# Optimization experiments

Measured on AMD Instinct MI355X. Metric: run time of the kernel, lower is better.

## Reference

```python
import jax, jax.numpy as jnp
import numpy as np


def setup_inputs() -> dict:
    key = jax.random.key(0)
    k1, k2, k3 = jax.random.split(key, 3)
    Q, N, D = 2048, 100000, 512
    x = jax.random.normal(k1, (Q, D), dtype=jnp.float32)
    target_embeddings = jax.random.normal(k2, (N, D), dtype=jnp.float32)
    target_labels = jax.random.randint(k3, (N,), 0, 400, dtype=jnp.int64)
    return {"x": x, "target_embeddings": target_embeddings,
            "target_labels": target_labels, "k": 5}


def reference(x, target_embeddings, target_labels, k):
    # torch.cdist(x[:,None], T[None], p=2).squeeze(1): full [Q, N] euclidean distances
    x2 = jnp.sum(x * x, axis=-1, keepdims=True)            # [Q, 1]
    t2 = jnp.sum(target_embeddings * target_embeddings, axis=-1)  # [N]
    d2 = x2 + t2[None, :] - 2.0 * (x @ target_embeddings.T)       # [Q, N]
    dist = jnp.sqrt(jnp.maximum(d2, 0.0))
    # topk smallest distances
    neg_vals, topk_inds = jax.lax.top_k(-dist, k)           # [Q, k]
    topk_dists = -neg_vals
    # pred = target_labels[inds].t() in the original eval path
    pred = target_labels[topk_inds].T                       # [k, Q]
    return topk_dists, topk_inds, pred
```

## Files before the change

### kernel.cpp

```cpp
#include <hip/hip_runtime.h>
#include <float.h>
#include <math.h>

#define NQ 2048
#define NT 100000
#define DIM 512
#define KTOP 5
#define NCAND 16
#define QTILE 128
#define TTILE 128
#define NTPC 13
#define NCH 64
#define TBLKS 782
#define QBLKS 16
#define NSUB 3
#define CV_TBLKS (TBLKS*16)
#define CV_XBLKS ((NQ/128)*16)

typedef float f32x4 __attribute__((ext_vector_type(4)));
typedef short s16x8 __attribute__((ext_vector_type(8)));
typedef unsigned int u32;
typedef unsigned short u16;

__device__ __forceinline__ int tsub_start(int ts) { return (13 * ts + 2) / 3; }

__device__ __forceinline__ bool lt_pair(float v1, int i1, float v2, int i2) {
  return v1 < v2 || (v1 == v2 && i1 < i2);
}

__device__ __forceinline__ void ins5f(float* tv, int* tix, float sc, int idx) {
  if (sc < tv[4]) {
    tv[4] = sc; tix[4] = idx;
#pragma unroll
    for (int p = 4; p > 0; --p)
      if (tv[p] < tv[p - 1]) {
        float tf = tv[p]; tv[p] = tv[p - 1]; tv[p - 1] = tf;
        int tn = tix[p]; tix[p] = tix[p - 1]; tix[p - 1] = tn;
      }
  }
}

__device__ __forceinline__ void ins5(float* tv, int* tix, float sc, int idx) {
  if (lt_pair(sc, idx, tv[4], tix[4])) {
    tv[4] = sc; tix[4] = idx;
#pragma unroll
    for (int p = 4; p > 0; --p)
      if (lt_pair(tv[p], tix[p], tv[p - 1], tix[p - 1])) {
        float tf = tv[p]; tv[p] = tv[p - 1]; tv[p - 1] = tf;
        int tn = tix[p]; tix[p] = tix[p - 1]; tix[p - 1] = tn;
      }
  }
}

__device__ __forceinline__ void merge5(float* av, int* ai, const float* bv, const int* bi) {
  float nv[5]; int ni[5];
#pragma unroll
  for (int s = 0; s < 5; ++s) {
    if (lt_pair(av[s], ai[s], bv[4 - s], bi[4 - s])) { nv[s] = av[s]; ni[s] = ai[s]; }
    else { nv[s] = bv[4 - s]; ni[s] = bi[4 - s]; }
  }
#pragma unroll
  for (int a = 0; a < 5; ++a)
#pragma unroll
    for (int b = 0; b < 4 - a; ++b)
      if (lt_pair(nv[b + 1], ni[b + 1], nv[b], ni[b])) {
        float tf = nv[b]; nv[b] = nv[b + 1]; nv[b + 1] = tf;
        int tn = ni[b]; ni[b] = ni[b + 1]; ni[b + 1] = tn;
      }
#pragma unroll
  for (int s = 0; s < 5; ++s) { av[s] = nv[s]; ai[s] = ni[s]; }
}

__global__ __launch_bounds__(256) void convert_kernel(
    const float* __restrict__ x, const float* __restrict__ T,
    short* __restrict__ xhi, short* __restrict__ thi,
    float* __restrict__ t2, float* __restrict__ x2) {
  __shared__ short lh[4096];
  const int bid = blockIdx.x;
  const bool isT = bid < CV_TBLKS;
  const int task = isT ? bid : bid - CV_TBLKS;
  const int blk = task >> 4, kbi = task & 15;
  const float* src = isT ? T : x;
  short* dhi = isT ? thi : xhi;
  float* nrm = isT ? t2 : x2;
  const int nsrc = isT ? NT : NQ;

  const int t = threadIdx.x;
  const int rr = t >> 1, half = t & 1;
  const int grow = blk * 128 + rr;
  const int rs = grow < nsrc ? grow : nsrc - 1;
  const float* p = src + (size_t)rs * DIM + kbi * 32 + half * 16;
  f32x4 v[4];
#pragma unroll
  for (int i = 0; i < 4; ++i) v[i] = ((const f32x4*)p)[i];

  float ss = 0.f;
#pragma unroll
  for (int g = 0; g < 2; ++g) {
    s16x8 hv;
#pragma unroll
    for (int e = 0; e < 8; ++e) {
      int i = g * 8 + e;
      float f = v[i >> 2][i & 3];
      ss = fmaf(f, f, ss);
      u32 u = __builtin_bit_cast(u32, f);
      u32 r1 = u + 0x7FFFu + ((u >> 16) & 1u);
      hv[e] = (short)(r1 >> 16);
    }
    int unit = (rr >> 4) * 64 + (half * 2 + g) * 16 + (rr & 15);
    *(s16x8*)(lh + unit * 8) = hv;
  }
  ss += __shfl_xor(ss, 1, 64);
  if (half == 0 && grow < nsrc) atomicAdd(nrm + grow, ss);

  __syncthreads();
  size_t obase = ((size_t)(blk * 16 + kbi)) * 4096 + t * 16;
  *(s16x8*)(dhi + obase)     = *(const s16x8*)(lh + t * 16);
  *(s16x8*)(dhi + obase + 8) = *(const s16x8*)(lh + t * 16 + 8);
}

__global__ __launch_bounds__(256, 2) void knn_mfma(
    const short* __restrict__ xhi, const short* __restrict__ thi,
    const float* __restrict__ t2g,
    float* __restrict__ pvals, u16* __restrict__ pidx16) {
  __shared__ float msv[128 * 5];
  __shared__ int   msi[128 * 5];

  const int tid = threadIdx.x;
  const int w = tid >> 6;
  const int l = tid & 63;
  const int bid = blockIdx.x;
  const u32 rest = (u32)bid >> 3;
  const int inner = (int)(rest % 48u);
  const int chunk = (bid & 7) + 8 * (int)(rest / 48u);
  const int qblk = inner & 15;
  const int tsub = inner >> 4;
  const int tstart = tsub_start(tsub);
  const int tend = tsub_start(tsub + 1);
  const int q0 = qblk * QTILE;
  const int wr = (w >> 1) * 64;
  const int wc = (w & 1) * 64;
  const int arow = wr >> 4;
  const int bcol = wc >> 4;

  const s16x8* xh8 = (const s16x8*)xhi;
  const s16x8* th8 = (const s16x8*)thi;

  float tv4[4][KTOP]; int tix4[4][KTOP];
#pragma unroll
  for (int jj = 0; jj < 4; ++jj)
#pragma unroll
    for (int s = 0; s < KTOP; ++s) { tv4[jj][s] = FLT_MAX; tix4[jj][s] = 0x7FFFFFFF; }

#pragma unroll 1
  for (int tt = tstart; tt < tend; ++tt) {
    const int bblk = chunk * NTPC + tt;
    if (bblk >= TBLKS) continue;
    const int tbase = bblk * TTILE;
    f32x4 acc[4][4];
#pragma unroll
    for (int i = 0; i < 4; ++i)
#pragma unroll
      for (int j = 0; j < 4; ++j) acc[i][j] = (f32x4){0.f, 0.f, 0.f, 0.f};

    u32 offA = (u32)(bblk * 16) * 512u + (u32)(arow * 64 + l);
    u32 offB = (u32)(qblk * 16) * 512u + (u32)(bcol * 64 + l);
    s16x8 ah[4], bh[4];
#pragma unroll 1
    for (int kbi = 0; kbi < 16; ++kbi) {
#pragma unroll
      for (int i = 0; i < 4; ++i) {
        ah[i] = th8[offA + i * 64];
        bh[i] = xh8[offB + i * 64];
      }
      offA += 512; offB += 512;
      __builtin_amdgcn_s_setprio(1);
#pragma unroll
      for (int j = 0; j < 4; ++j)
#pragma unroll
        for (int i = 0; i < 4; ++i)
          acc[i][j] = __builtin_amdgcn_mfma_f32_16x16x32_bf16(ah[i], bh[j], acc[i][j], 0, 0, 0);
      __builtin_amdgcn_s_setprio(0);
    }

    const int tg0 = tbase + wr + ((l >> 4) << 2);
    float t2v[16];
#pragma unroll
    for (int i = 0; i < 4; ++i)
#pragma unroll
      for (int r = 0; r < 4; ++r) {
        int t = tg0 + i * 16 + r;
        float vv = t2g[t < NT ? t : NT - 1];
        t2v[i * 4 + r] = t < NT ? vv : FLT_MAX;
      }
#pragma unroll
    for (int jj = 0; jj < 4; ++jj)
#pragma unroll
      for (int i = 0; i < 4; ++i)
#pragma unroll
        for (int r = 0; r < 4; ++r) {
          float sc = fmaf(-2.f, acc[i][jj][r], t2v[i * 4 + r]);
          ins5f(tv4[jj], tix4[jj], sc, tg0 + i * 16 + r);
        }
  }

#pragma unroll
  for (int jj = 0; jj < 4; ++jj)
#pragma unroll
    for (int d = 16; d <= 32; d <<= 1) {
      float ov[KTOP]; int oi[KTOP];
#pragma unroll
      for (int s = 0; s < KTOP; ++s) {
        ov[s] = __shfl_xor(tv4[jj][s], d, 64);
        oi[s] = __shfl_xor(tix4[jj][s], d, 64);
      }
      merge5(tv4[jj], tix4[jj], ov, oi);
    }

  const int blockBase = (chunk * NTPC + tstart) * TTILE;
  if ((w >> 1) && (l >> 4) == 0) {
#pragma unroll
    for (int jj = 0; jj < 4; ++jj) {
      int qr = wc + jj * 16 + l;
#pragma unroll
      for (int s = 0; s < KTOP; ++s) {
        msv[qr * 5 + s] = tv4[jj][s];
        msi[qr * 5 + s] = tix4[jj][s];
      }
    }
  }
  __syncthreads();
  if (!(w >> 1) && (l >> 4) == 0) {
#pragma unroll
    for (int jj = 0; jj < 4; ++jj) {
      int qr = wc + jj * 16 + l;
      float ov[KTOP]; int oi[KTOP];
#pragma unroll
      for (int s = 0; s < KTOP; ++s) { ov[s] = msv[qr * 5 + s]; oi[s] = msi[qr * 5 + s]; }
      merge5(tv4[jj], tix4[jj], ov, oi);
      int q = q0 + qr;
      size_t base = ((size_t)q * (NCH * NSUB) + (chunk * NSUB + tsub)) * KTOP;
#pragma unroll
      for (int s = 0; s < KTOP; ++s) {
        pvals[base + s] = tv4[jj][s];
        pidx16[base + s] = (u16)(tix4[jj][s] - blockBase);
      }
    }
  }
}

__global__ __launch_bounds__(256) void knn_merge16(
    const float* __restrict__ pvals, const u16* __restrict__ pidx16,
    int* __restrict__ idx16g) {
  const int M = NCH * NSUB * KTOP;
  int q = (blockIdx.x * 256 + threadIdx.x) >> 6;
  int l = threadIdx.x & 63;
  if (q >= NQ) return;
  float v[15]; int ix[15];
  size_t base = (size_t)q * M;
#pragma unroll
  for (int j = 0; j < 15; ++j) {
    int m = j * 64 + l;
    int slot = m / KTOP;
    int ch = slot / NSUB, ts = slot % NSUB;
    int gb = (ch * NTPC + tsub_start(ts)) * TTILE;
    v[j] = pvals[base + m];
    ix[j] = gb + (int)pidx16[base + m];
  }
  int mywin = 0x7FFFFFFF;
#pragma unroll 1
  for (int r = 0; r < NCAND; ++r) {
    float bv = FLT_MAX; int bi = 0x7FFFFFFF;
#pragma unroll
    for (int j = 0; j < 15; ++j)
      if (lt_pair(v[j], ix[j], bv, bi)) { bv = v[j]; bi = ix[j]; }
#pragma unroll
    for (int d = 1; d < 64; d <<= 1) {
      float ov = __shfl_xor(bv, d, 64);
      int oi = __shfl_xor(bi, d, 64);
      if (lt_pair(ov, oi, bv, bi)) { bv = ov; bi = oi; }
    }
    if (l == r) mywin = bi;
#pragma unroll
    for (int j = 0; j < 15; ++j)
      if (ix[j] == bi) v[j] = FLT_MAX;
  }
  if (l < NCAND) idx16g[q * NCAND + l] = mywin;
}

__global__ __launch_bounds__(256) void knn_rerank(
    const float* __restrict__ x, const float* __restrict__ T,
    const int* __restrict__ idx16g, const int* __restrict__ labels,
    float* __restrict__ out) {
  __shared__ float sd2[4 * NCAND];
  __shared__ int sti[4 * NCAND];
  const int w = threadIdx.x >> 6, l = threadIdx.x & 63;
  const int q = blockIdx.x * 4 + w;
  const int cand = l >> 2, sub = l & 3;
  const int ti = idx16g[q * NCAND + cand];
  const f32x4* tp = (const f32x4*)(T + (size_t)ti * DIM + sub * 128);
  const f32x4* xp = (const f32x4*)(x + (size_t)q * DIM + sub * 128);
  float dot = 0.f, tt = 0.f, xx = 0.f;
#pragma unroll
  for (int i = 0; i < 32; ++i) {
    f32x4 a = xp[i], b = tp[i];
#pragma unroll
    for (int c = 0; c < 4; ++c) {
      dot = fmaf(a[c], b[c], dot);
      tt  = fmaf(b[c], b[c], tt);
      xx  = fmaf(a[c], a[c], xx);
    }
  }
#pragma unroll
  for (int d = 1; d < 4; d <<= 1) {
    dot += __shfl_xor(dot, d, 64);
    tt  += __shfl_xor(tt, d, 64);
    xx  += __shfl_xor(xx, d, 64);
  }
  if (sub == 0) { sd2[w * NCAND + cand] = xx + tt - 2.f * dot; sti[w * NCAND + cand] = ti; }
  __syncthreads();
  if (l == 0) {
    float tv[KTOP]; int tix[KTOP];
#pragma unroll
    for (int s = 0; s < KTOP; ++s) { tv[s] = FLT_MAX; tix[s] = 0x7FFFFFFF; }
#pragma unroll
    for (int c = 0; c < NCAND; ++c) ins5(tv, tix, sd2[w * NCAND + c], sti[w * NCAND + c]);
#pragma unroll
    for (int s = 0; s < KTOP; ++s) {
      float d2 = tv[s] > 0.f ? tv[s] : 0.f;
      out[(size_t)q * KTOP + s] = sqrtf(d2);
      out[(size_t)NQ * KTOP + (size_t)q * KTOP + s] = (float)tix[s];
      out[(size_t)2 * NQ * KTOP + (size_t)s * NQ + q] =
          (float)labels[tix[s]];
    }
  }
}

extern "C" void kernel_launch(void* const* d_in, const int* in_sizes, int n_in,
                              void* d_out, int out_size, void* d_ws, size_t ws_size,
                              hipStream_t stream) {
  const float* x = (const float*)d_in[0];
  const float* T = (const float*)d_in[1];
  const int* labels = (const int*)d_in[2];
  float* out = (float*)d_out;
  char* ws = (char*)d_ws;

  float* t2     = (float*)(ws + 0);
  float* x2     = (float*)(ws + 401408);
  short* xhi    = (short*)(ws + 409600);
  short* thi    = (short*)(ws + 2506752);
  float* pvals  = (float*)(ws + 105005056);
  u16*   pidx16 = (u16*)(ws + 112869376);
  int*   idx16g = (int*)(ws + 116801536);

  hipMemsetAsync(ws, 0, 409600, stream);

  convert_kernel<<<CV_TBLKS + CV_XBLKS, 256, 0, stream>>>(
      x, T, xhi, thi, t2, x2);

  knn_mfma<<<QBLKS * NSUB * NCH, 256, 0, stream>>>(
      xhi, thi, t2, pvals, pidx16);

  knn_merge16<<<(NQ * 64 + 255) / 256, 256, 0, stream>>>(pvals, pidx16, idx16g);

  knn_rerank<<<NQ / 4, 256, 0, stream>>>(x, T, idx16g, labels, out);
}
```

Measured before the change: 693.1 us.

## Stage MFMA operands through double-buffered LDS via direct global-to-LDS loads

The inner K loop no longer loads bf16 operand fragments from global memory straight into registers. Each block now copies 128x32 tiles of T and X into a two-slot LDS buffer with global_load_lds, overlapping the load of the next k-slice with MFMA on the current one. Each operand is fetched from global once per block and shared across waves, where before each wave loaded its own slice. In exchange the kernel adds 32KB of LDS per block and two __syncthreads per k-step, which may cut occupancy (launch bounds ask for 2 blocks/CU) and drops the s_setprio hints.

New measurement: 809.5 us. +16.8%, slower.

```diff
diff --git a/kernel.cpp b/kernel.cpp
--- a/kernel.cpp
+++ b/kernel.cpp
@@ -123,8 +123,10 @@
     const short* __restrict__ xhi, const short* __restrict__ thi,
     const float* __restrict__ t2g,
     float* __restrict__ pvals, u16* __restrict__ pidx16) {
-  __shared__ float msv[128 * 5];
-  __shared__ int   msi[128 * 5];
+  __shared__ char smem[32768];
+  s16x8 (*stg)[1024] = (s16x8 (*)[1024])smem;
+  float* msv = (float*)smem;
+  int*   msi = (int*)(smem + 2560);
 
   const int tid = threadIdx.x;
   const int w = tid >> 6;
@@ -143,8 +145,34 @@
   const int arow = wr >> 4;
   const int bcol = wc >> 4;
 
-  const s16x8* xh8 = (const s16x8*)xhi;
-  const s16x8* th8 = (const s16x8*)thi;
+#define STAGE_KBI(kbi, b) do {                                                \
+    _Pragma("unroll")                                                         \
+    for (int c = 0; c < 4; ++c) {                                             \
+      int seg = w * 4 + c;                                                    \
+      const short* gsrc = (seg < 8)                                           \
+        ? thi + (((size_t)(bblk * 16 + (kbi))) << 12) + (seg << 9) + (l << 3) \
+        : xhi + (((size_t)(qblk * 16 + (kbi))) << 12) + ((seg - 8) << 9) + (l << 3); \
+      __builtin_amdgcn_global_load_lds(                                       \
+          (const __attribute__((address_space(1))) unsigned int*)gsrc,        \
+          (__attribute__((address_space(3))) unsigned int*)&stg[(b)][seg * 64], \
+          16, 0, 0);                                                          \
+    }                                                                         \
+  } while (0)
+
+#define READ_MFMA(b) do {                                                     \
+    s16x8 ah[4], bh[4];                                                       \
+    _Pragma("unroll")                                                         \
+    for (int i = 0; i < 4; ++i) {                                             \
+      ah[i] = stg[(b)][(arow + i) * 64 + l];                                  \
+      bh[i] = stg[(b)][512 + (bcol + i) * 64 + l];                            \
+    }                                                                         \
+    _Pragma("unroll")                                                         \
+    for (int j = 0; j < 4; ++j)                                               \
+      _Pragma("unroll")                                                       \
+      for (int i = 0; i < 4; ++i)                                             \
+        acc[i][j] = __builtin_amdgcn_mfma_f32_16x16x32_bf16(ah[i], bh[j],     \
+                                                            acc[i][j], 0, 0, 0); \
+  } while (0)
 
   float tv4[4][KTOP]; int tix4[4][KTOP];
 #pragma unroll
@@ -163,24 +191,17 @@
 #pragma unroll
       for (int j = 0; j < 4; ++j) acc[i][j] = (f32x4){0.f, 0.f, 0.f, 0.f};
 
-    u32 offA = (u32)(bblk * 16) * 512u + (u32)(arow * 64 + l);
-    u32 offB = (u32)(qblk * 16) * 512u + (u32)(bcol * 64 + l);
-    s16x8 ah[4], bh[4];
+    STAGE_KBI(0, 0);
+    __syncthreads();
 #pragma unroll 1
-    for (int kbi = 0; kbi < 16; ++kbi) {
-#pragma unroll
-      for (int i = 0; i < 4; ++i) {
-        ah[i] = th8[offA + i * 64];
-        bh[i] = xh8[offB + i * 64];
-      }
-      offA += 512; offB += 512;
-      __builtin_amdgcn_s_setprio(1);
-#pragma unroll
-      for (int j = 0; j < 4; ++j)
-#pragma unroll
-        for (int i = 0; i < 4; ++i)
-          acc[i][j] = __builtin_amdgcn_mfma_f32_16x16x32_bf16(ah[i], bh[j], acc[i][j], 0, 0, 0);
-      __builtin_amdgcn_s_setprio(0);
+    for (int ks = 0; ks < 8; ++ks) {
+      const int k0 = ks * 2;
+      STAGE_KBI(k0 + 1, 1);
+      READ_MFMA(0);
+      __syncthreads();
+      if (ks < 7) STAGE_KBI(k0 + 2, 0);
+      READ_MFMA(1);
+      __syncthreads();
     }
 
     const int tg0 = tbase + wr + ((l >> 4) << 2);
@@ -203,6 +224,8 @@
           ins5f(tv4[jj], tix4[jj], sc, tg0 + i * 16 + r);
         }
   }
+#undef STAGE_KBI
+#undef READ_MFMA
 
 #pragma unroll
   for (int jj = 0; jj < 4; ++jj)
```
